# Optimization experiments

Hardware: AMD Instinct MI355X
Metric: run time of the kernel (lower is better)

The kernel has to match this reference:

```python
import jax, jax.numpy as jnp
import numpy as np

B, IN, HID, LAT, EH = 32768, 512, 2048, 128, 512
MID = max(HID // 2, LAT * 2)      # 1024
HALF = max(EH // 2, 4)            # 256
EPS = 1e-5
LN10 = float(np.log(10.0))


def setup_inputs() -> dict:
    key = jax.random.key(0)
    ks = jax.random.split(key, 24)
    r = lambda k, shp, s=0.02: (jax.random.normal(k, shp, dtype=jnp.float32) * s)
    d = {
        "x": jax.random.normal(ks[0], (B, IN), dtype=jnp.float32),
        "group_idx": jax.random.randint(ks[1], (B,), 0, 3),
        # encoder: Linear(IN,HID)+BN+ELU, Linear(HID,MID)+BN+ELU, Linear(MID,LAT)
        "e_w1": r(ks[2], (HID, IN)), "e_b1": jnp.zeros((HID,), jnp.float32),
        "e_g1": jnp.ones((HID,), jnp.float32), "e_be1": jnp.zeros((HID,), jnp.float32),
        "e_w2": r(ks[3], (MID, HID)), "e_b2": jnp.zeros((MID,), jnp.float32),
        "e_g2": jnp.ones((MID,), jnp.float32), "e_be2": jnp.zeros((MID,), jnp.float32),
        "e_w3": r(ks[4], (LAT, MID)), "e_b3": jnp.zeros((LAT,), jnp.float32),
        # shared: Linear(LAT+IN,HID)+BN+ELU, Linear(HID,MID)+BN+ELU
        "s_w1": r(ks[5], (HID, LAT + IN)), "s_b1": jnp.zeros((HID,), jnp.float32),
        "s_g1": jnp.ones((HID,), jnp.float32), "s_be1": jnp.zeros((HID,), jnp.float32),
        "s_w2": r(ks[6], (MID, HID)), "s_b2": jnp.zeros((MID,), jnp.float32),
        "s_g2": jnp.ones((MID,), jnp.float32), "s_be2": jnp.zeros((MID,), jnp.float32),
        # 3 expert heads, stacked on leading axis E=3
        "h_w1": r(ks[7], (3, EH, MID)), "h_b1": jnp.zeros((3, EH), jnp.float32),
        "h_w2": r(ks[8], (3, HALF, EH)), "h_b2": jnp.zeros((3, HALF), jnp.float32),
        "h_w3": r(ks[9], (3, HALF)), "h_b3": jnp.zeros((3,), jnp.float32),
    }
    return d


def _bn(h, g, b):
    # BatchNorm1d in training mode: batch mean, biased batch var
    m = jnp.mean(h, axis=0)
    v = jnp.var(h, axis=0)
    return (h - m) * (g / jnp.sqrt(v + EPS)) + b


def _elu(h):
    return jax.nn.elu(h)


def reference(x, group_idx,
              e_w1, e_b1, e_g1, e_be1, e_w2, e_b2, e_g2, e_be2, e_w3, e_b3,
              s_w1, s_b1, s_g1, s_be1, s_w2, s_b2, s_g2, s_be2,
              h_w1, h_b1, h_w2, h_b2, h_w3, h_b3):
    # encoder
    h = _elu(_bn(x @ e_w1.T + e_b1, e_g1, e_be1))
    h = _elu(_bn(h @ e_w2.T + e_b2, e_g2, e_be2))
    latent = h @ e_w3.T + e_b3                              # [B, LAT]
    # shared trunk
    z = jnp.concatenate([latent, x], axis=-1)               # [B, LAT+IN]
    h = _elu(_bn(z @ s_w1.T + s_b1, s_g1, s_be1))
    hidden = _elu(_bn(h @ s_w2.T + s_b2, s_g2, s_be2))      # [B, MID]
    # expert heads: compute all 3 (tiny vs trunk), then select per-row group
    t1 = _elu(jnp.einsum('bm,ehm->ebh', hidden, h_w1) + h_b1[:, None, :])   # [3,B,EH]
    t2 = _elu(jnp.einsum('ebh,efh->ebf', t1, h_w2) + h_b2[:, None, :])      # [3,B,HALF]
    pred_all = jnp.einsum('ebf,ef->eb', t2, h_w3) + h_b3[:, None]           # [3,B]
    pred_raw = jnp.take_along_axis(pred_all, group_idx[None, :], axis=0)[0] # [B]
    pred_log = -jax.nn.softplus(pred_raw)
    pred_prob = jnp.exp(pred_log * jnp.float32(LN10))       # 10 ** pred_log
    return pred_log, pred_prob
```

## Files before the change

kernel.cpp:

```cpp
#include <hip/hip_runtime.h>
#include <math.h>

#define B_    32768
#define LN10_ 2.302585092994046f
#define MT_H  264
#define NBLK  128

typedef __attribute__((ext_vector_type(8))) short short8;
typedef __attribute__((ext_vector_type(4))) float f32x4;

typedef const __attribute__((address_space(1))) void gvoid_t;
typedef __attribute__((address_space(3))) void svoid_t;

__device__ __forceinline__ void gl16(const void* g, void* l) {
  __builtin_amdgcn_global_load_lds((gvoid_t*)g, (svoid_t*)l, 16, 0, 0);
}

__device__ __forceinline__ float bf2f(unsigned int u) {
  union { unsigned int i; float f; } v; v.i = u << 16; return v.f;
}
__device__ __forceinline__ unsigned short f2bf(float f) {
  union { float f; unsigned int i; } v; v.f = f;
  unsigned int x = v.i;
  unsigned int r = x + 0x7FFFu + ((x >> 16) & 1u);
  return (unsigned short)(r >> 16);
}

#define TLA 16384

__global__ __launch_bounds__(512)
void gemm256(const unsigned short* __restrict__ A0, int lda,
             const unsigned short* __restrict__ W0, int ldw,
             unsigned short* __restrict__ C0, int ldc, int K,
             float* __restrict__ st, int Ntot) {
  __shared__ __align__(16) unsigned short lds[4 * TLA];
  const int t = threadIdx.x;
  const int nx = gridDim.x, ny = gridDim.y;
  const int f = blockIdx.y * nx + blockIdx.x;
  const int xcd = f & 7, g = f >> 3;
  const int gdiv = g / nx;
  const int mt = xcd * (ny >> 3) + gdiv;
  const int nt = g - gdiv * nx;
  const int mBase = mt * 256, nBase = nt * 256;
  const unsigned short* Ap = A0 + (size_t)mBase * lda;
  const unsigned short* Wp = W0 + (size_t)nBase * ldw;
  const int w = t >> 6, l = t & 63;
  const int wr = w >> 2, wc = w & 3;
  const int lm = l & 15, lg = l >> 4;

  const int rr = t >> 3;
  const int xc = ((t & 7) ^ (rr & 7)) << 3;
  const unsigned short* gA = Ap + (size_t)rr * lda + xc;
  const unsigned short* gB = Wp + (size_t)rr * ldw + xc;

#define STAGE_A(tt)                                                       \
  {                                                                       \
    const int d_ = ((tt) & 1) * 2 * TLA;                                  \
    const size_t ko_ = (size_t)(tt) * 64;                                 \
    gl16(gA + ko_,                    &lds[d_ + t * 8]);                  \
    gl16(gA + (size_t)64 * lda + ko_, &lds[d_ + 4096 + t * 8]);           \
    gl16(gA + (size_t)128 * lda + ko_, &lds[d_ + 8192 + t * 8]);          \
    gl16(gA + (size_t)192 * lda + ko_, &lds[d_ + 12288 + t * 8]);         \
  }
#define STAGE_B(tt)                                                       \
  {                                                                       \
    const int d_ = ((tt) & 1) * 2 * TLA + TLA;                            \
    const size_t ko_ = (size_t)(tt) * 64;                                 \
    gl16(gB + ko_,                    &lds[d_ + t * 8]);                  \
    gl16(gB + (size_t)64 * ldw + ko_, &lds[d_ + 4096 + t * 8]);           \
    gl16(gB + (size_t)128 * ldw + ko_, &lds[d_ + 8192 + t * 8]);          \
    gl16(gB + (size_t)192 * ldw + ko_, &lds[d_ + 12288 + t * 8]);         \
  }

  const int cs0 = ((lg) ^ (l & 7)) << 3;
  const int cs1 = ((4 | lg) ^ (l & 7)) << 3;

  f32x4 acc[8][4];
#pragma unroll
  for (int i = 0; i < 8; ++i)
#pragma unroll
    for (int j = 0; j < 4; ++j) {
      f32x4 z4 = {0.f, 0.f, 0.f, 0.f};
      acc[i][j] = z4;
    }

  const int NT = K >> 6;
  STAGE_A(0); STAGE_B(0);

  for (int tt = 0; tt < NT; ++tt) {
    asm volatile("s_waitcnt vmcnt(0)" ::: "memory");
    __builtin_amdgcn_s_barrier();
    __builtin_amdgcn_sched_barrier(0);
    const int d = (tt & 1) * 2 * TLA;
    const bool more = (tt + 1 < NT);
    if (more) STAGE_A(tt + 1);
    {
      short8 af[8], bq[4];
#pragma unroll
      for (int i = 0; i < 8; ++i) {
        int arow = wr * 128 + i * 16 + lm;
        af[i] = *(const short8*)&lds[d + arow * 64 + cs0];
      }
#pragma unroll
      for (int j = 0; j < 4; ++j) {
        int brow = wc * 64 + j * 16 + lm;
        bq[j] = *(const short8*)&lds[d + TLA + brow * 64 + cs0];
      }
      __builtin_amdgcn_s_setprio(1);
#pragma unroll
      for (int i = 0; i < 8; ++i)
#pragma unroll
        for (int j = 0; j < 4; ++j)
          acc[i][j] = __builtin_amdgcn_mfma_f32_16x16x32_bf16(af[i], bq[j], acc[i][j], 0, 0, 0);
      __builtin_amdgcn_s_setprio(0);
    }
    if (more) STAGE_B(tt + 1);
    {
      short8 af[8], bq[4];
#pragma unroll
      for (int i = 0; i < 8; ++i) {
        int arow = wr * 128 + i * 16 + lm;
        af[i] = *(const short8*)&lds[d + arow * 64 + cs1];
      }
#pragma unroll
      for (int j = 0; j < 4; ++j) {
        int brow = wc * 64 + j * 16 + lm;
        bq[j] = *(const short8*)&lds[d + TLA + brow * 64 + cs1];
      }
      __builtin_amdgcn_s_setprio(1);
#pragma unroll
      for (int i = 0; i < 8; ++i)
#pragma unroll
        for (int j = 0; j < 4; ++j)
          acc[i][j] = __builtin_amdgcn_mfma_f32_16x16x32_bf16(af[i], bq[j], acc[i][j], 0, 0, 0);
      __builtin_amdgcn_s_setprio(0);
    }
  }

#pragma unroll
  for (int j = 0; j < 4; ++j) {
    int n = nBase + wc * 64 + j * 16 + lm;
    float s1 = 0.f, q1 = 0.f;
#pragma unroll
    for (int i = 0; i < 8; ++i) {
      int m0 = mBase + wr * 128 + i * 16 + lg * 4;
#pragma unroll
      for (int r = 0; r < 4; ++r) {
        float v = acc[i][j][r];
        s1 += v; q1 += v * v;
        C0[(size_t)(m0 + r) * ldc + n] = f2bf(v);
      }
    }
    s1 += __shfl_xor(s1, 16, 64); s1 += __shfl_xor(s1, 32, 64);
    q1 += __shfl_xor(q1, 16, 64); q1 += __shfl_xor(q1, 32, 64);
    if (lg == 0) { atomicAdd(&st[n], s1); atomicAdd(&st[Ntot + n], q1); }
  }
}
#undef STAGE_A
#undef STAGE_B

__global__ __launch_bounds__(256)
void gemm_bt(const unsigned short* __restrict__ A0, int lda,
             const unsigned short* __restrict__ W0, int ldw,
             unsigned short* __restrict__ C0, int ldc,
             int K, const float* __restrict__ bias0, int elu,
             float* __restrict__ st, int Ntot,
             long eA, long eW, long eC, int eBias,
             const int* __restrict__ texp) {
  __shared__ __align__(16) unsigned short lA[128 * 64];
  __shared__ __align__(16) unsigned short lB[128 * 64];
  const int t = threadIdx.x;
  const int nx = gridDim.x, ny = gridDim.y;
  const int f = blockIdx.y * nx + blockIdx.x;
  const int xcd = f & 7, g = f >> 3;
  const int gdiv = g / nx;
  const int mt = xcd * (ny >> 3) + gdiv;
  const int nt = g - gdiv * nx;
  const int mBase = mt * 128;
  const int nBase = nt * 128;
  int e = texp ? texp[mt] : (int)blockIdx.z;
  if (e < 0) return;
  const unsigned short* A = A0 + (size_t)e * eA;
  const unsigned short* W = W0 + (size_t)e * eW;
  unsigned short* C = C0 + (size_t)e * eC;
  const float* bias = bias0 ? (bias0 + (size_t)e * eBias) : nullptr;
  const unsigned short* Ap = A + (size_t)mBase * lda;
  const unsigned short* Wp = W + (size_t)nBase * ldw;
  const int w = t >> 6, l = t & 63;
  const int wr = (w >> 1) * 64, wc = (w & 1) * 64;
  const int lm = l & 15, lg = l >> 4;

  f32x4 acc[4][4];
#pragma unroll
  for (int i = 0; i < 4; ++i)
#pragma unroll
    for (int j = 0; j < 4; ++j) {
      f32x4 z4 = {0.f, 0.f, 0.f, 0.f};
      acc[i][j] = z4;
    }

  for (int k0 = 0; k0 < K; k0 += 64) {
    __syncthreads();
#pragma unroll
    for (int it = 0; it < 4; ++it) {
      int chunk = it * 256 + t;
      int row = chunk >> 3, sc = chunk & 7;
      int gc = (sc ^ (row & 7)) << 3;
      gl16(Ap + (size_t)row * lda + k0 + gc, &lA[chunk * 8]);
      gl16(Wp + (size_t)row * ldw + k0 + gc, &lB[chunk * 8]);
    }
    __syncthreads();
#pragma unroll
    for (int kk = 0; kk < 64; kk += 32) {
      short8 af[4], bfr[4];
#pragma unroll
      for (int i = 0; i < 4; ++i) {
        int ar = wr + i * 16 + lm;
        int ac = (kk >> 3) + lg;
        af[i] = *(const short8*)&lA[ar * 64 + ((ac ^ (ar & 7)) << 3)];
      }
#pragma unroll
      for (int j = 0; j < 4; ++j) {
        int br = wc + j * 16 + lm;
        int bc = (kk >> 3) + lg;
        bfr[j] = *(const short8*)&lB[br * 64 + ((bc ^ (br & 7)) << 3)];
      }
#pragma unroll
      for (int i = 0; i < 4; ++i)
#pragma unroll
        for (int j = 0; j < 4; ++j)
          acc[i][j] = __builtin_amdgcn_mfma_f32_16x16x32_bf16(af[i], bfr[j], acc[i][j], 0, 0, 0);
    }
  }

#pragma unroll
  for (int j = 0; j < 4; ++j) {
    int n = nBase + wc + j * 16 + lm;
    float bj = bias ? bias[n] : 0.f;
    float s = 0.f, q = 0.f;
#pragma unroll
    for (int i = 0; i < 4; ++i) {
      int m0 = mBase + wr + i * 16 + lg * 4;
#pragma unroll
      for (int r = 0; r < 4; ++r) {
        float v = acc[i][j][r] + bj;
        if (elu) v = v > 0.f ? v : expm1f(v);
        s += v; q += v * v;
        C[(size_t)(m0 + r) * ldc + n] = f2bf(v);
      }
    }
    if (st) {
      s += __shfl_xor(s, 16, 64); s += __shfl_xor(s, 32, 64);
      q += __shfl_xor(q, 16, 64); q += __shfl_xor(q, 32, 64);
      if (lg == 0) { atomicAdd(&st[n], s); atomicAdd(&st[Ntot + n], q); }
    }
  }
}

__global__ void bn_apply(unsigned short* __restrict__ Y, const float* __restrict__ st,
                         const float* __restrict__ gam, const float* __restrict__ bet,
                         int N, float invB) {
  size_t i = (size_t)blockIdx.x * blockDim.x + threadIdx.x;
  size_t base = i * 8;
  int col = (int)(base & (size_t)(N - 1));
  float a8[8], b8[8];
#pragma unroll
  for (int k = 0; k < 8; ++k) {
    int c = col + k;
    float m = st[c] * invB;
    float var = st[N + c] * invB - m * m;
    float av = gam[c] * rsqrtf(var + 1e-5f);
    a8[k] = av;
    b8[k] = bet[c] - m * av;
  }
  uint4 u = *(uint4*)&Y[base];
  unsigned int uu[4] = {u.x, u.y, u.z, u.w};
  unsigned int oo[4];
#pragma unroll
  for (int k = 0; k < 4; ++k) {
    float vlo = bf2f(uu[k] & 0xFFFFu);
    float vhi = bf2f(uu[k] >> 16);
    float flo = a8[2 * k] * vlo + b8[2 * k];
    float fhi = a8[2 * k + 1] * vhi + b8[2 * k + 1];
    flo = flo > 0.f ? flo : expm1f(flo);
    fhi = fhi > 0.f ? fhi : expm1f(fhi);
    oo[k] = (unsigned int)f2bf(flo) | ((unsigned int)f2bf(fhi) << 16);
  }
  uint4 o = {oo[0], oo[1], oo[2], oo[3]};
  *(uint4*)&Y[base] = o;
}

__global__ void cast_all(const float* __restrict__ e1, const float* __restrict__ e2,
                         const float* __restrict__ e3, const float* __restrict__ s1,
                         const float* __restrict__ s2, const float* __restrict__ h1,
                         const float* __restrict__ h2, unsigned short* __restrict__ dst) {
  int i4 = blockIdx.x * 256 + threadIdx.x;
  const float* src;
  int rel;
  if (i4 < 786432) {
    if (i4 < 262144) { src = e1; rel = i4; }
    else             { src = e2; rel = i4 - 262144; }
  } else if (i4 < 1146880) {
    if (i4 < 819200) { src = e3; rel = i4 - 786432; }
    else             { src = s1; rel = i4 - 819200; }
  } else if (i4 < 2064384) {
    if (i4 < 1671168) { src = s2; rel = i4 - 1146880; }
    else              { src = h1; rel = i4 - 1671168; }
  } else { src = h2; rel = i4 - 2064384; }
  float4 v = ((const float4*)src)[rel];
  ushort4 o = {f2bf(v.x), f2bf(v.y), f2bf(v.z), f2bf(v.w)};
  ((ushort4*)dst)[i4] = o;
}

__global__ void cast_x(const float* __restrict__ x, unsigned short* __restrict__ z) {
  int i = blockIdx.x * blockDim.x + threadIdx.x;
  int b = i >> 7;
  int c = (i & 127) << 2;
  float4 v = *(const float4*)&x[(size_t)b * 512 + c];
  ushort4 o = {f2bf(v.x), f2bf(v.y), f2bf(v.z), f2bf(v.w)};
  *(ushort4*)&z[(size_t)b * 640 + 128 + c] = o;
}

__global__ void hist_blocks(const int* __restrict__ gidx, int* __restrict__ bcnt) {
  int blk = blockIdx.x;
  int i = blk * 256 + threadIdx.x;
  int e = gidx[i];
  int l = threadIdx.x & 63, w = threadIdx.x >> 6;
  __shared__ int wc[4][3];
  unsigned long long m0 = __ballot(e == 0);
  unsigned long long m1 = __ballot(e == 1);
  unsigned long long m2 = __ballot(e == 2);
  if (l == 0) { wc[w][0] = __popcll(m0); wc[w][1] = __popcll(m1); wc[w][2] = __popcll(m2); }
  __syncthreads();
  if (threadIdx.x < 3)
    bcnt[blk * 3 + threadIdx.x] = wc[0][threadIdx.x] + wc[1][threadIdx.x] +
                                  wc[2][threadIdx.x] + wc[3][threadIdx.x];
}

__global__ void scan_plan(const int* __restrict__ bcnt, int* __restrict__ boff,
                          int* __restrict__ vend, int* __restrict__ texp) {
  __shared__ int sp[4];
  __shared__ int cnt[3];
  int t = threadIdx.x;
  if (t < 3) {
    int s = 0;
    for (int b = 0; b < NBLK; ++b) s += bcnt[b * 3 + t];
    cnt[t] = s;
  }
  __syncthreads();
  if (t == 0) {
    int p = 0;
    for (int e = 0; e < 3; ++e) {
      sp[e] = p; vend[e] = p + cnt[e];
      p += ((cnt[e] + 127) >> 7) << 7;
    }
    sp[3] = p;
  }
  __syncthreads();
  if (t < 3) {
    int run = sp[t];
    for (int b = 0; b < NBLK; ++b) { boff[b * 3 + t] = run; run += bcnt[b * 3 + t]; }
  }
  if (t < MT_H) {
    int r0 = t << 7, e = -1;
    for (int k = 0; k < 3; ++k)
      if (r0 >= sp[k] && r0 < sp[k + 1]) e = k;
    texp[t] = e;
  }
}

__global__ void scatter2(const int* __restrict__ gidx, const int* __restrict__ boff,
                         int* __restrict__ perm) {
  int blk = blockIdx.x;
  int i = blk * 256 + threadIdx.x;
  int e = gidx[i];
  int l = threadIdx.x & 63, w = threadIdx.x >> 6;
  __shared__ int wc[4][3];
  unsigned long long m0 = __ballot(e == 0);
  unsigned long long m1 = __ballot(e == 1);
  unsigned long long m2 = __ballot(e == 2);
  if (l == 0) { wc[w][0] = __popcll(m0); wc[w][1] = __popcll(m1); wc[w][2] = __popcll(m2); }
  __syncthreads();
  unsigned long long me = (e == 0) ? m0 : ((e == 1) ? m1 : m2);
  int rank = __popcll(me & ((1ull << l) - 1ull));
  int woff = 0;
  for (int ww = 0; ww < w; ++ww) woff += wc[ww][e];
  perm[boff[blk * 3 + e] + woff + rank] = i;
}

__global__ void gather_h(const unsigned short* __restrict__ hid, const int* __restrict__ perm,
                         const int* __restrict__ texp, const int* __restrict__ vend,
                         unsigned short* __restrict__ ht) {
  int idx = blockIdx.x * 256 + threadIdx.x;
  int p = idx >> 7, c8 = (idx & 127) << 3;
  int e = texp[p >> 7];
  uint4 v = {0u, 0u, 0u, 0u};
  if (e >= 0 && p < vend[e]) {
    int src = perm[p];
    v = *(const uint4*)&hid[(size_t)src * 1024 + c8];
  }
  *(uint4*)&ht[(size_t)p * 1024 + c8] = v;
}

__global__ void final_pred(const unsigned short* __restrict__ t2, const int* __restrict__ perm,
                           const int* __restrict__ texp, const int* __restrict__ vend,
                           const float* __restrict__ w3, const float* __restrict__ b3,
                           float* __restrict__ out) {
  int p = blockIdx.x * 4 + (threadIdx.x >> 6);
  int l = threadIdx.x & 63;
  int e = texp[p >> 7];
  if (e < 0 || p >= vend[e]) return;
  ushort4 u = *(const ushort4*)&t2[(size_t)p * 256 + l * 4];
  float4 wv = *(const float4*)&w3[e * 256 + l * 4];
  float sum = bf2f(u.x) * wv.x + bf2f(u.y) * wv.y + bf2f(u.z) * wv.z + bf2f(u.w) * wv.w;
#pragma unroll
  for (int off = 32; off; off >>= 1) sum += __shfl_down(sum, off, 64);
  if (l == 0) {
    int orig = perm[p];
    float xr = sum + b3[e];
    float sp = (xr > 0.f) ? (xr + log1pf(expf(-xr))) : log1pf(expf(xr));
    float pl = -sp;
    out[orig] = pl;
    out[B_ + orig] = expf(pl * LN10_);
  }
}

extern "C" void kernel_launch(void* const* d_in, const int* in_sizes, int n_in,
                              void* d_out, int out_size, void* d_ws, size_t ws_size,
                              hipStream_t stream) {
  const float* x    = (const float*)d_in[0];
  const int*   gidx = (const int*)d_in[1];
  const float* e_w1 = (const float*)d_in[2];
  const float* e_g1 = (const float*)d_in[4];
  const float* e_be1= (const float*)d_in[5];
  const float* e_w2 = (const float*)d_in[6];
  const float* e_g2 = (const float*)d_in[8];
  const float* e_be2= (const float*)d_in[9];
  const float* e_w3 = (const float*)d_in[10];
  const float* e_b3 = (const float*)d_in[11];
  const float* s_w1 = (const float*)d_in[12];
  const float* s_g1 = (const float*)d_in[14];
  const float* s_be1= (const float*)d_in[15];
  const float* s_w2 = (const float*)d_in[16];
  const float* s_g2 = (const float*)d_in[18];
  const float* s_be2= (const float*)d_in[19];
  const float* h_w1 = (const float*)d_in[20];
  const float* h_b1 = (const float*)d_in[21];
  const float* h_w2 = (const float*)d_in[22];
  const float* h_b2 = (const float*)d_in[23];
  const float* h_w3 = (const float*)d_in[24];
  const float* h_b3 = (const float*)d_in[25];
  float* out = (float*)d_out;

  char* ws = (char*)d_ws;
  size_t off = 0;
  auto alloc = [&](size_t bytes) -> char* {
    char* p = ws + off;
    off += (bytes + 255) & ~(size_t)255;
    return p;
  };
  unsigned short* wb_e1 = (unsigned short*)alloc((size_t)2048 * 512 * 2);
  unsigned short* wb_e2 = (unsigned short*)alloc((size_t)1024 * 2048 * 2);
  unsigned short* wb_e3 = (unsigned short*)alloc((size_t)128 * 1024 * 2);
  unsigned short* wb_s1 = (unsigned short*)alloc((size_t)2048 * 640 * 2);
  unsigned short* wb_s2 = (unsigned short*)alloc((size_t)1024 * 2048 * 2);
  unsigned short* wb_h1 = (unsigned short*)alloc((size_t)3 * 512 * 1024 * 2);
  unsigned short* wb_h2 = (unsigned short*)alloc((size_t)3 * 256 * 512 * 2);
  unsigned short* z     = (unsigned short*)alloc((size_t)B_ * 640 * 2);
  unsigned short* bufA  = (unsigned short*)alloc((size_t)B_ * 2048 * 2);
  unsigned short* bufB  = (unsigned short*)alloc((size_t)B_ * 1024 * 2);
  float* st = (float*)alloc(12288 * sizeof(float));
  float* st0 = st;
  float* st1 = st + 4096;
  float* st2 = st + 6144;
  float* st3 = st + 10240;
  int* bcnt = (int*)alloc(NBLK * 3 * sizeof(int));
  int* boff = (int*)alloc(NBLK * 3 * sizeof(int));
  int* vend = (int*)alloc(3 * sizeof(int));
  int* texp = (int*)alloc(MT_H * sizeof(int));
  int* perm = (int*)alloc((size_t)MT_H * 128 * sizeof(int));
  unsigned short* ht  = bufA;
  unsigned short* t1p = bufA + (size_t)MT_H * 128 * 1024;
  unsigned short* t2p = z;

  cast_all<<<8448, 256, 0, stream>>>(e_w1, e_w2, e_w3, s_w1, s_w2, h_w1, h_w2, wb_e1);
  cast_x<<<(B_ * 128) / 256, 256, 0, stream>>>(x, z);
  hipMemsetAsync(st, 0, 12288 * sizeof(float), stream);
  hist_blocks<<<NBLK, 256, 0, stream>>>(gidx, bcnt);
  scan_plan<<<1, 512, 0, stream>>>(bcnt, boff, vend, texp);
  scatter2<<<NBLK, 256, 0, stream>>>(gidx, boff, perm);

  gemm256<<<dim3(8, 128), 512, 0, stream>>>(z + 128, 640, wb_e1, 512, bufA, 2048, 512,
                                            st0, 2048);
  bn_apply<<<B_, 256, 0, stream>>>(bufA, st0, e_g1, e_be1, 2048, 1.0f / B_);
  gemm256<<<dim3(4, 128), 512, 0, stream>>>(bufA, 2048, wb_e2, 2048, bufB, 1024, 2048,
                                            st1, 1024);
  bn_apply<<<B_ / 2, 256, 0, stream>>>(bufB, st1, e_g2, e_be2, 1024, 1.0f / B_);
  gemm_bt<<<dim3(1, 256), 256, 0, stream>>>(bufB, 1024, wb_e3, 1024, z, 640, 1024,
                                            e_b3, 0, nullptr, 0, 0, 0, 0, 0, nullptr);
  gemm256<<<dim3(8, 128), 512, 0, stream>>>(z, 640, wb_s1, 640, bufA, 2048, 640,
                                            st2, 2048);
  bn_apply<<<B_, 256, 0, stream>>>(bufA, st2, s_g1, s_be1, 2048, 1.0f / B_);
  gemm256<<<dim3(4, 128), 512, 0, stream>>>(bufA, 2048, wb_s2, 2048, bufB, 1024, 2048,
                                            st3, 1024);
  bn_apply<<<B_ / 2, 256, 0, stream>>>(bufB, st3, s_g2, s_be2, 1024, 1.0f / B_);

  gather_h<<<(MT_H * 128 * 128) / 256, 256, 0, stream>>>(bufB, perm, texp, vend, ht);

  gemm_bt<<<dim3(4, MT_H), 256, 0, stream>>>(ht, 1024, wb_h1, 1024, t1p, 512, 1024,
                                             h_b1, 1, nullptr, 0,
                                             0, (long)512 * 1024, 0, 512, texp);
  gemm_bt<<<dim3(2, MT_H), 256, 0, stream>>>(t1p, 512, wb_h2, 512, t2p, 256, 512,
                                             h_b2, 1, nullptr, 0,
                                             0, (long)256 * 512, 0, 256, texp);

  final_pred<<<(MT_H * 128) / 4, 256, 0, stream>>>(t2p, perm, texp, vend, h_w3, h_b3, out);
}
```

Baseline: 1.025 ms.

## Split gemm256 mainloop into four interleaved load/MFMA phases with partial waits

Reworks the 256x256 bf16 GEMM main loop so each K-tile is handled in four sub-phases. Each phase stages one quarter of the next tile's A/B data with global_load_lds and runs one quarter of the MFMAs, using vmcnt(2) partial waits and extra barriers in place of a single full drain per tile. The B-tile column mapping per wave changes to match the halved B loads, and the epilogue column index is updated to suit. The goal is to overlap global-to-LDS traffic with MFMA work and shorten register live ranges, at the cost of more barriers per iteration.

```diff
diff --git a/kernel.cpp b/kernel.cpp
--- a/kernel.cpp
+++ b/kernel.cpp
@@ -26,14 +26,14 @@
   return (unsigned short)(r >> 16);
 }
 
-#define TLA 16384
+#define HLF 8192
 
 __global__ __launch_bounds__(512)
-void gemm256(const unsigned short* __restrict__ A0, int lda,
-             const unsigned short* __restrict__ W0, int ldw,
+void gemm256(const unsigned short* __restrict__ A0_, int lda,
+             const unsigned short* __restrict__ W0_, int ldw,
              unsigned short* __restrict__ C0, int ldc, int K,
              float* __restrict__ st, int Ntot) {
-  __shared__ __align__(16) unsigned short lds[4 * TLA];
+  __shared__ __align__(16) unsigned short lds[65536];
   const int t = threadIdx.x;
   const int nx = gridDim.x, ny = gridDim.y;
   const int f = blockIdx.y * nx + blockIdx.x;
@@ -42,8 +42,8 @@
   const int mt = xcd * (ny >> 3) + gdiv;
   const int nt = g - gdiv * nx;
   const int mBase = mt * 256, nBase = nt * 256;
-  const unsigned short* Ap = A0 + (size_t)mBase * lda;
-  const unsigned short* Wp = W0 + (size_t)nBase * ldw;
+  const unsigned short* Ap = A0_ + (size_t)mBase * lda;
+  const unsigned short* Wp = W0_ + (size_t)nBase * ldw;
   const int w = t >> 6, l = t & 63;
   const int wr = w >> 2, wc = w & 3;
   const int lm = l & 15, lg = l >> 4;
@@ -53,24 +53,16 @@
   const unsigned short* gA = Ap + (size_t)rr * lda + xc;
   const unsigned short* gB = Wp + (size_t)rr * ldw + xc;
 
-#define STAGE_A(tt)                                                       \
-  {                                                                       \
-    const int d_ = ((tt) & 1) * 2 * TLA;                                  \
-    const size_t ko_ = (size_t)(tt) * 64;                                 \
-    gl16(gA + ko_,                    &lds[d_ + t * 8]);                  \
-    gl16(gA + (size_t)64 * lda + ko_, &lds[d_ + 4096 + t * 8]);           \
-    gl16(gA + (size_t)128 * lda + ko_, &lds[d_ + 8192 + t * 8]);          \
-    gl16(gA + (size_t)192 * lda + ko_, &lds[d_ + 12288 + t * 8]);         \
-  }
-#define STAGE_B(tt)                                                       \
-  {                                                                       \
-    const int d_ = ((tt) & 1) * 2 * TLA + TLA;                            \
-    const size_t ko_ = (size_t)(tt) * 64;                                 \
-    gl16(gB + ko_,                    &lds[d_ + t * 8]);                  \
-    gl16(gB + (size_t)64 * ldw + ko_, &lds[d_ + 4096 + t * 8]);           \
-    gl16(gB + (size_t)128 * ldw + ko_, &lds[d_ + 8192 + t * 8]);          \
-    gl16(gB + (size_t)192 * ldw + ko_, &lds[d_ + 12288 + t * 8]);         \
-  }
+#define SG(ptr, ld, rowoff, dst) \
+    gl16((ptr) + (size_t)(rowoff) * (ld) + ko_, &lds[(dst) + t * 8])
+#define STAGE_A0(tt) { const int d_=((tt)&1)<<15; const size_t ko_=(size_t)(tt)*64; \
+    SG(gA,lda,0,d_);          SG(gA,lda,64,d_+4096); }
+#define STAGE_A1(tt) { const int d_=((tt)&1)<<15; const size_t ko_=(size_t)(tt)*64; \
+    SG(gA,lda,128,d_+8192);   SG(gA,lda,192,d_+12288); }
+#define STAGE_B0(tt) { const int d_=((tt)&1)<<15; const size_t ko_=(size_t)(tt)*64; \
+    SG(gB,ldw,0,d_+16384);    SG(gB,ldw,64,d_+20480); }
+#define STAGE_B1(tt) { const int d_=((tt)&1)<<15; const size_t ko_=(size_t)(tt)*64; \
+    SG(gB,ldw,128,d_+24576);  SG(gB,ldw,192,d_+28672); }
 
   const int cs0 = ((lg) ^ (l & 7)) << 3;
   const int cs1 = ((4 | lg) ^ (l & 7)) << 3;
@@ -85,61 +77,89 @@
     }
 
   const int NT = K >> 6;
-  STAGE_A(0); STAGE_B(0);
-
+  STAGE_A0(0); STAGE_A1(0); STAGE_B0(0); STAGE_B1(0);
+  asm volatile("s_waitcnt vmcnt(2)" ::: "memory");
+  __builtin_amdgcn_s_barrier();
+
+  short8 af[8], bq[4];
   for (int tt = 0; tt < NT; ++tt) {
-    asm volatile("s_waitcnt vmcnt(0)" ::: "memory");
-    __builtin_amdgcn_s_barrier();
+    const int d = (tt & 1) << 15;
+    const bool more = (tt + 1 < NT);
+    const int abase = d + wr * HLF + lm * 64;
+    const int bbase = d + 2 * HLF + (wc * 32 + lm) * 64;
+#pragma unroll
+    for (int i = 0; i < 8; ++i) af[i] = *(const short8*)&lds[abase + i * 1024 + cs0];
+    bq[0] = *(const short8*)&lds[bbase + cs0];
+    bq[1] = *(const short8*)&lds[bbase + 1024 + cs0];
+    if (more) {
+      STAGE_A0(tt + 1);
+      asm volatile("s_waitcnt vmcnt(2)" ::: "memory");
+    } else {
+      asm volatile("s_waitcnt vmcnt(0)" ::: "memory");
+    }
+    __builtin_amdgcn_s_barrier();
+    asm volatile("s_waitcnt lgkmcnt(0)" ::: "memory");
     __builtin_amdgcn_sched_barrier(0);
-    const int d = (tt & 1) * 2 * TLA;
-    const bool more = (tt + 1 < NT);
-    if (more) STAGE_A(tt + 1);
-    {
-      short8 af[8], bq[4];
-#pragma unroll
-      for (int i = 0; i < 8; ++i) {
-        int arow = wr * 128 + i * 16 + lm;
-        af[i] = *(const short8*)&lds[d + arow * 64 + cs0];
-      }
-#pragma unroll
-      for (int j = 0; j < 4; ++j) {
-        int brow = wc * 64 + j * 16 + lm;
-        bq[j] = *(const short8*)&lds[d + TLA + brow * 64 + cs0];
-      }
-      __builtin_amdgcn_s_setprio(1);
-#pragma unroll
-      for (int i = 0; i < 8; ++i)
-#pragma unroll
-        for (int j = 0; j < 4; ++j)
-          acc[i][j] = __builtin_amdgcn_mfma_f32_16x16x32_bf16(af[i], bq[j], acc[i][j], 0, 0, 0);
-      __builtin_amdgcn_s_setprio(0);
-    }
-    if (more) STAGE_B(tt + 1);
-    {
-      short8 af[8], bq[4];
-#pragma unroll
-      for (int i = 0; i < 8; ++i) {
-        int arow = wr * 128 + i * 16 + lm;
-        af[i] = *(const short8*)&lds[d + arow * 64 + cs1];
-      }
-#pragma unroll
-      for (int j = 0; j < 4; ++j) {
-        int brow = wc * 64 + j * 16 + lm;
-        bq[j] = *(const short8*)&lds[d + TLA + brow * 64 + cs1];
-      }
-      __builtin_amdgcn_s_setprio(1);
-#pragma unroll
-      for (int i = 0; i < 8; ++i)
-#pragma unroll
-        for (int j = 0; j < 4; ++j)
-          acc[i][j] = __builtin_amdgcn_mfma_f32_16x16x32_bf16(af[i], bq[j], acc[i][j], 0, 0, 0);
-      __builtin_amdgcn_s_setprio(0);
-    }
+    __builtin_amdgcn_s_setprio(1);
+#pragma unroll
+    for (int i = 0; i < 8; ++i) {
+      acc[i][0] = __builtin_amdgcn_mfma_f32_16x16x32_bf16(af[i], bq[0], acc[i][0], 0, 0, 0);
+      acc[i][1] = __builtin_amdgcn_mfma_f32_16x16x32_bf16(af[i], bq[1], acc[i][1], 0, 0, 0);
+    }
+    __builtin_amdgcn_s_setprio(0);
+    __builtin_amdgcn_s_barrier();
+    bq[2] = *(const short8*)&lds[bbase + HLF + cs0];
+    bq[3] = *(const short8*)&lds[bbase + HLF + 1024 + cs0];
+    if (more) STAGE_A1(tt + 1);
+    __builtin_amdgcn_s_barrier();
+    asm volatile("s_waitcnt lgkmcnt(0)" ::: "memory");
+    __builtin_amdgcn_sched_barrier(0);
+    __builtin_amdgcn_s_setprio(1);
+#pragma unroll
+    for (int i = 0; i < 8; ++i) {
+      acc[i][2] = __builtin_amdgcn_mfma_f32_16x16x32_bf16(af[i], bq[2], acc[i][2], 0, 0, 0);
+      acc[i][3] = __builtin_amdgcn_mfma_f32_16x16x32_bf16(af[i], bq[3], acc[i][3], 0, 0, 0);
+    }
+    __builtin_amdgcn_s_setprio(0);
+    __builtin_amdgcn_s_barrier();
+#pragma unroll
+    for (int i = 0; i < 8; ++i) af[i] = *(const short8*)&lds[abase + i * 1024 + cs1];
+    bq[0] = *(const short8*)&lds[bbase + cs1];
+    bq[1] = *(const short8*)&lds[bbase + 1024 + cs1];
+    if (more) STAGE_B0(tt + 1);
+    __builtin_amdgcn_s_barrier();
+    asm volatile("s_waitcnt lgkmcnt(0)" ::: "memory");
+    __builtin_amdgcn_sched_barrier(0);
+    __builtin_amdgcn_s_setprio(1);
+#pragma unroll
+    for (int i = 0; i < 8; ++i) {
+      acc[i][0] = __builtin_amdgcn_mfma_f32_16x16x32_bf16(af[i], bq[0], acc[i][0], 0, 0, 0);
+      acc[i][1] = __builtin_amdgcn_mfma_f32_16x16x32_bf16(af[i], bq[1], acc[i][1], 0, 0, 0);
+    }
+    __builtin_amdgcn_s_setprio(0);
+    __builtin_amdgcn_s_barrier();
+    bq[2] = *(const short8*)&lds[bbase + HLF + cs1];
+    bq[3] = *(const short8*)&lds[bbase + HLF + 1024 + cs1];
+    if (more) {
+      STAGE_B1(tt + 1);
+      asm volatile("s_waitcnt vmcnt(2)" ::: "memory");
+    }
+    __builtin_amdgcn_s_barrier();
+    asm volatile("s_waitcnt lgkmcnt(0)" ::: "memory");
+    __builtin_amdgcn_sched_barrier(0);
+    __builtin_amdgcn_s_setprio(1);
+#pragma unroll
+    for (int i = 0; i < 8; ++i) {
+      acc[i][2] = __builtin_amdgcn_mfma_f32_16x16x32_bf16(af[i], bq[2], acc[i][2], 0, 0, 0);
+      acc[i][3] = __builtin_amdgcn_mfma_f32_16x16x32_bf16(af[i], bq[3], acc[i][3], 0, 0, 0);
+    }
+    __builtin_amdgcn_s_setprio(0);
+    __builtin_amdgcn_s_barrier();
   }
 
 #pragma unroll
   for (int j = 0; j < 4; ++j) {
-    int n = nBase + wc * 64 + j * 16 + lm;
+    int n = nBase + (j >> 1) * 128 + wc * 32 + (j & 1) * 16 + lm;
     float s1 = 0.f, q1 = 0.f;
 #pragma unroll
     for (int i = 0; i < 8; ++i) {
@@ -156,8 +176,11 @@
     if (lg == 0) { atomicAdd(&st[n], s1); atomicAdd(&st[Ntot + n], q1); }
   }
 }
-#undef STAGE_A
-#undef STAGE_B
+#undef SG
+#undef STAGE_A0
+#undef STAGE_A1
+#undef STAGE_B0
+#undef STAGE_B1
 
 __global__ __launch_bounds__(256)
 void gemm_bt(const unsigned short* __restrict__ A0, int lda,
```

Result: no change. 1.006 ms (-1.9%).
